# Kernel optimization log

Hardware: AMD Instinct MI355X
Metric: run time of the kernel (lower is better)

The kernel has to match this reference:

```python
import jax, jax.numpy as jnp
import numpy as np

HIDDEN = 1024
HEADS = 16
HEAD_DIM = HIDDEN // HEADS


def setup_inputs() -> dict:
    key = jax.random.key(0)
    ks = jax.random.split(key, 12)
    B, S, D = 2, 2048, HIDDEN
    scale = 1.0 / np.sqrt(D)
    return {
        "query": jax.random.normal(ks[0], (B, S, D), jnp.float32),
        "key": jax.random.normal(ks[1], (B, S, D), jnp.float32),
        "value": jax.random.normal(ks[2], (B, S, D), jnp.float32),
        "Wq": jax.random.normal(ks[3], (D, D), jnp.float32) * scale,
        "bq": jnp.zeros((D,), jnp.float32),
        "Wk": jax.random.normal(ks[4], (D, D), jnp.float32) * scale,
        "bk": jnp.zeros((D,), jnp.float32),
        "Wv": jax.random.normal(ks[5], (D, D), jnp.float32) * scale,
        "bv": jnp.zeros((D,), jnp.float32),
        "Wo": jax.random.normal(ks[6], (D, D), jnp.float32) * scale,
        "bo": jnp.zeros((D,), jnp.float32),
    }


def reference(query, key, value, Wq, bq, Wk, bk, Wv, bv, Wo, bo):
    B, S, D = query.shape
    H, Hd = HEADS, HEAD_DIM
    sm_scale = 1.0 / jnp.sqrt(jnp.asarray(Hd, query.dtype))

    def proj(x, W, b):  # nn.Linear: x @ W.T + b, then split heads -> [B,H,S,Hd]
        y = jnp.einsum("bsd,ed->bse", x, W) + b
        return y.reshape(B, S, H, Hd).transpose(0, 2, 1, 3)

    Q = proj(query, Wq, bq)
    K = proj(key, Wk, bk)
    V = proj(value, Wv, bv)

    scores = jnp.einsum("bhqd,bhkd->bhqk", Q, K) * sm_scale  # [B,H,S,S]
    attn = jax.nn.softmax(scores, axis=-1)
    ctx = jnp.einsum("bhqk,bhkd->bhqd", attn, V)
    ctx = ctx.transpose(0, 2, 1, 3).reshape(B, S, D)
    out = jnp.einsum("bsd,ed->bse", ctx, Wo) + bo
    return out
```

## Files before the change

kernel.cpp:

```cpp
#include <hip/hip_runtime.h>
#include <stdint.h>

typedef unsigned short u16;
typedef unsigned int u32;
typedef __attribute__((ext_vector_type(8))) short s16x8;
typedef __attribute__((ext_vector_type(4))) float fx4;

#define AS_GLOBAL __attribute__((address_space(1)))
#define AS_LDS    __attribute__((address_space(3)))

__device__ __forceinline__ void g2l16(const u16* g, u16* l) {
  __builtin_amdgcn_global_load_lds((const AS_GLOBAL unsigned int*)g,
                                   (AS_LDS unsigned int*)l, 16, 0, 0);
}
__device__ __forceinline__ u16 f2bf(float f) {
  u32 u = __float_as_uint(f);
  u += 0x7FFF + ((u >> 16) & 1);
  return (u16)(u >> 16);
}
__device__ __forceinline__ u32 pkcvt(float a, float b) {
  u32 r;
  asm("v_cvt_pk_bf16_f32 %0, %1, %2" : "=v"(r) : "v"(a), "v"(b));
  return r;
}

__global__ __launch_bounds__(256) void cvt3(const float* __restrict__ a, const float* __restrict__ b,
                                            const float* __restrict__ c, u16* oa, u16* ob, u16* oc, int n4) {
  const float* src = blockIdx.y == 0 ? a : blockIdx.y == 1 ? b : c;
  u16* dst = blockIdx.y == 0 ? oa : blockIdx.y == 1 ? ob : oc;
  int i = blockIdx.x * 256 + threadIdx.x;
  if (i >= n4) return;
  float4 f = ((const float4*)src)[i];
  ushort4 o; o.x = f2bf(f.x); o.y = f2bf(f.y); o.z = f2bf(f.z); o.w = f2bf(f.w);
  ((ushort4*)dst)[i] = o;
}
__global__ __launch_bounds__(256) void cvt4(const float* __restrict__ a, const float* __restrict__ b,
                                            const float* __restrict__ c, const float* __restrict__ d,
                                            u16* oa, u16* ob, u16* oc, u16* od, int n4) {
  const float* src = blockIdx.y == 0 ? a : blockIdx.y == 1 ? b : blockIdx.y == 2 ? c : d;
  u16* dst = blockIdx.y == 0 ? oa : blockIdx.y == 1 ? ob : blockIdx.y == 2 ? oc : od;
  int i = blockIdx.x * 256 + threadIdx.x;
  if (i >= n4) return;
  float4 f = ((const float4*)src)[i];
  ushort4 o; o.x = f2bf(f.x); o.y = f2bf(f.y); o.z = f2bf(f.z); o.w = f2bf(f.w);
  ((ushort4*)dst)[i] = o;
}

__global__ __launch_bounds__(256) void gemm_qkv(
    const u16* __restrict__ Aq, const u16* __restrict__ Ak, const u16* __restrict__ Av,
    const u16* __restrict__ Wq, const u16* __restrict__ Wk, const u16* __restrict__ Wv,
    const float* __restrict__ bq, const float* __restrict__ bk, const float* __restrict__ bv,
    u16* __restrict__ Oq, u16* __restrict__ Ok, u16* __restrict__ Ovt)
{
  constexpr int K = 1024;
  __shared__ u16 As[128 * 32];
  __shared__ u16 Bs[128 * 32];
  const int z = blockIdx.z;
  const u16* A = z == 0 ? Aq : z == 1 ? Ak : Av;
  const u16* W = z == 0 ? Wq : z == 1 ? Wk : Wv;
  const float* bias = z == 0 ? bq : z == 1 ? bk : bv;
  const float scale = z == 0 ? 0.180336880f : 1.0f;

  const int bm = blockIdx.x, bn = blockIdx.y;
  const int tid = threadIdx.x;
  const int lane = tid & 63, wave = tid >> 6;
  const int quad = lane >> 4, col = lane & 15;
  const int wm = wave >> 1, wn = wave & 1;

  const int L0 = tid, L1 = 256 + tid;
  const int r0 = L0 >> 2, c0 = (L0 & 3) ^ ((r0 >> 1) & 3);
  const int r1 = L1 >> 2, c1 = (L1 & 3) ^ ((r1 >> 1) & 3);
  const u16* gA0 = A + (bm * 128 + r0) * K + c0 * 8;
  const u16* gA1 = A + (bm * 128 + r1) * K + c1 * 8;
  const u16* gB0 = W + (bn * 128 + r0) * K + c0 * 8;
  const u16* gB1 = W + (bn * 128 + r1) * K + c1 * 8;
  u16* lA0 = As + L0 * 8; u16* lA1 = As + L1 * 8;
  u16* lB0 = Bs + L0 * 8; u16* lB1 = Bs + L1 * 8;

  const int aRow = wm * 64 + col;
  const int bRow = wn * 64 + col;

  fx4 zero = {0.f, 0.f, 0.f, 0.f};
  fx4 acc[4][4];
#pragma unroll
  for (int i = 0; i < 4; ++i)
#pragma unroll
    for (int j = 0; j < 4; ++j) acc[i][j] = zero;

  for (int kb = 0; kb < K / 32; ++kb) {
    __syncthreads();
    g2l16(gA0 + kb * 32, lA0);
    g2l16(gA1 + kb * 32, lA1);
    g2l16(gB0 + kb * 32, lB0);
    g2l16(gB1 + kb * 32, lB1);
    __syncthreads();
    s16x8 af[4], bf[4];
#pragma unroll
    for (int mt = 0; mt < 4; ++mt) {
      int row = aRow + mt * 16;
      int ch = row * 4 + (quad ^ ((row >> 1) & 3));
      af[mt] = *(const s16x8*)(As + ch * 8);
    }
#pragma unroll
    for (int nt = 0; nt < 4; ++nt) {
      int row = bRow + nt * 16;
      int ch = row * 4 + (quad ^ ((row >> 1) & 3));
      bf[nt] = *(const s16x8*)(Bs + ch * 8);
    }
#pragma unroll
    for (int mt = 0; mt < 4; ++mt)
#pragma unroll
      for (int nt = 0; nt < 4; ++nt)
        acc[mt][nt] = __builtin_amdgcn_mfma_f32_16x16x32_bf16(af[mt], bf[nt], acc[mt][nt], 0, 0, 0);
  }

  if (z == 2) {
#pragma unroll
    for (int nt = 0; nt < 4; ++nt) {
      int n = bn * 128 + wn * 64 + nt * 16 + col;
      float bvv = bias[n];
      int h = n >> 6, hd = n & 63;
#pragma unroll
      for (int mt = 0; mt < 4; ++mt) {
        int mbase = bm * 128 + wm * 64 + mt * 16 + quad * 4;
        int b = mbase >> 11, s = mbase & 2047;
        uint2 w;
        w.x = pkcvt(acc[mt][nt][0] + bvv, acc[mt][nt][1] + bvv);
        w.y = pkcvt(acc[mt][nt][2] + bvv, acc[mt][nt][3] + bvv);
        *(uint2*)(Ovt + ((size_t)((b * 16 + h) * 64 + hd)) * 2048 + s) = w;
      }
    }
  } else {
    u16* outB = z == 0 ? Oq : Ok;
#pragma unroll
    for (int nt = 0; nt < 4; ++nt) {
      int n = bn * 128 + wn * 64 + nt * 16 + col;
      float bvv = bias[n];
#pragma unroll
      for (int mt = 0; mt < 4; ++mt) {
        int mbase = bm * 128 + wm * 64 + mt * 16 + quad * 4;
#pragma unroll
        for (int reg = 0; reg < 4; ++reg) {
          int m = mbase + reg;
          float v = (acc[mt][nt][reg] + bvv) * scale;
          int b = m >> 11, s = m & 2047;
          int h = n >> 6, hd = n & 63;
          outB[((b * 16 + h) * 2048 + s) * 64 + hd] = f2bf(v);
        }
      }
    }
  }
}

__global__ __launch_bounds__(256) void gemm_out(
    const u16* __restrict__ A, const u16* __restrict__ W,
    const float* __restrict__ bias, float* __restrict__ outF)
{
  constexpr int K = 1024;
  __shared__ u16 As[128 * 32];
  __shared__ u16 Bs[64 * 32];
  const int bm = blockIdx.x, bn = blockIdx.y;
  const int tid = threadIdx.x;
  const int lane = tid & 63, wave = tid >> 6;
  const int quad = lane >> 4, col = lane & 15;
  const int wm = wave >> 1, wn = wave & 1;

  const int L0 = tid, L1 = 256 + tid;
  const int r0 = L0 >> 2, c0 = (L0 & 3) ^ ((r0 >> 1) & 3);
  const int r1 = L1 >> 2, c1 = (L1 & 3) ^ ((r1 >> 1) & 3);
  const u16* gA0 = A + (bm * 128 + r0) * K + c0 * 8;
  const u16* gA1 = A + (bm * 128 + r1) * K + c1 * 8;
  const u16* gB0 = W + (bn * 64 + r0) * K + c0 * 8;
  u16* lA0 = As + L0 * 8; u16* lA1 = As + L1 * 8;
  u16* lB0 = Bs + L0 * 8;

  const int aRow = wm * 64 + col;
  const int bRow = wn * 32 + col;

  fx4 zero = {0.f, 0.f, 0.f, 0.f};
  fx4 acc[4][2];
#pragma unroll
  for (int i = 0; i < 4; ++i)
#pragma unroll
    for (int j = 0; j < 2; ++j) acc[i][j] = zero;

  for (int kb = 0; kb < K / 32; ++kb) {
    __syncthreads();
    g2l16(gA0 + kb * 32, lA0);
    g2l16(gA1 + kb * 32, lA1);
    g2l16(gB0 + kb * 32, lB0);
    __syncthreads();
    s16x8 af[4], bf[2];
#pragma unroll
    for (int mt = 0; mt < 4; ++mt) {
      int row = aRow + mt * 16;
      int ch = row * 4 + (quad ^ ((row >> 1) & 3));
      af[mt] = *(const s16x8*)(As + ch * 8);
    }
#pragma unroll
    for (int nt = 0; nt < 2; ++nt) {
      int row = bRow + nt * 16;
      int ch = row * 4 + (quad ^ ((row >> 1) & 3));
      bf[nt] = *(const s16x8*)(Bs + ch * 8);
    }
#pragma unroll
    for (int mt = 0; mt < 4; ++mt)
#pragma unroll
      for (int nt = 0; nt < 2; ++nt)
        acc[mt][nt] = __builtin_amdgcn_mfma_f32_16x16x32_bf16(af[mt], bf[nt], acc[mt][nt], 0, 0, 0);
  }

#pragma unroll
  for (int nt = 0; nt < 2; ++nt) {
    int n = bn * 64 + wn * 32 + nt * 16 + col;
    float bvv = bias[n];
#pragma unroll
    for (int mt = 0; mt < 4; ++mt) {
      int mbase = bm * 128 + wm * 64 + mt * 16 + quad * 4;
#pragma unroll
      for (int reg = 0; reg < 4; ++reg)
        outF[(mbase + reg) * 1024 + n] = acc[mt][nt][reg] + bvv;
    }
  }
}

__global__ __launch_bounds__(512, 4) void flash_attn(
    const u16* __restrict__ Qp, const u16* __restrict__ Kp,
    const u16* __restrict__ Vt, u16* __restrict__ ctx)
{
  __shared__ u16 sh[32768];
  const int qt = blockIdx.x, bh = blockIdx.y;
  const int tid = threadIdx.x, lane = tid & 63, wave = tid >> 6;
  const int quad = lane >> 4, col = lane & 15;
  const int wm = wave >> 1, wn = wave & 1;

  const u16* Qb = Qp + ((size_t)bh * 2048 + qt * 128) * 64;
  const u16* Kb = Kp + (size_t)bh * 2048 * 64;
  const u16* Vb = Vt + (size_t)bh * 64 * 2048;

  s16x8 qf[2][2];
#pragma unroll
  for (int mt = 0; mt < 2; ++mt)
#pragma unroll
    for (int h = 0; h < 2; ++h)
      qf[mt][h] = *(const s16x8*)(Qb + (wm * 32 + mt * 16 + col) * 64 + h * 32 + quad * 8);

  fx4 zero = {0.f, 0.f, 0.f, 0.f};
  fx4 acc_o[2][4], acc_l[2];
#pragma unroll
  for (int mt = 0; mt < 2; ++mt) {
    acc_l[mt] = zero;
#pragma unroll
    for (int dt = 0; dt < 4; ++dt) acc_o[mt][dt] = zero;
  }
  s16x8 ones;
#pragma unroll
  for (int j = 0; j < 8; ++j) ones[j] = (short)0x3F80;

  u16* Vs = sh;
  u16* Ks = sh + 8192;
  u16* Pw = sh + 16384 + wave * 2048;

  const u16* vsrc[2];
#pragma unroll
  for (int i = 0; i < 2; ++i) {
    int d = wave * 8 + i * 4 + (lane >> 4);
    int cs = (lane & 15) ^ (d & 15);
    vsrc[i] = Vb + d * 2048 + cs * 8;
  }

  const u16* ksrc[2];
  u16* kdst[2];
#pragma unroll
  for (int i = 0; i < 2; ++i) {
    int idx = wave * 128 + i * 64 + lane;
    int d = idx >> 3, c = idx & 7;
    ksrc[i] = Kb + d * 64 + (c ^ (d & 7)) * 8;
    kdst[i] = Ks + (wave * 128 + i * 64) * 8;
  }

#pragma unroll
  for (int i = 0; i < 2; ++i) g2l16(ksrc[i], kdst[i]);
  asm volatile("s_waitcnt vmcnt(0)" ::: "memory");

  for (int kv = 0; kv < 16; ++kv) {
    const int n0 = kv * 128;
    __builtin_amdgcn_s_barrier();
#pragma unroll
    for (int i = 0; i < 2; ++i)
      g2l16(vsrc[i] + n0, Vs + (wave * 8 + i * 4) * 128);

    __builtin_amdgcn_s_setprio(1);
#pragma unroll
    for (int nt = 0; nt < 4; ++nt) {
      const int r = wn * 64 + nt * 16 + col;
      const u16* krow = Ks + r * 64;
      const int x = r & 7;
      s16x8 k0 = *(const s16x8*)(krow + ((quad ^ x) << 3));
      s16x8 k1 = *(const s16x8*)(krow + (((4 ^ quad) ^ x) << 3));
#pragma unroll
      for (int mt = 0; mt < 2; ++mt) {
        fx4 s = __builtin_amdgcn_mfma_f32_16x16x32_bf16(k0, qf[mt][0], zero, 0, 0, 0);
        s = __builtin_amdgcn_mfma_f32_16x16x32_bf16(k1, qf[mt][1], s, 0, 0, 0);
        int m = mt * 16 + col;
        int cch = 2 * nt + (quad >> 1);
        uint2 w;
        w.x = pkcvt(exp2f(s[0]), exp2f(s[1]));
        w.y = pkcvt(exp2f(s[2]), exp2f(s[3]));
        *(uint2*)(Pw + m * 64 + ((cch ^ (m & 7))) * 8 + (quad & 1) * 4) = w;
      }
    }
    __builtin_amdgcn_s_setprio(0);

    asm volatile("s_waitcnt vmcnt(0)" ::: "memory");
    asm volatile("s_waitcnt lgkmcnt(0)" ::: "memory");
    __builtin_amdgcn_s_barrier();

    if (kv < 15) {
#pragma unroll
      for (int i = 0; i < 2; ++i)
        g2l16(ksrc[i] + (kv + 1) * 8192, kdst[i]);
    }

    __builtin_amdgcn_s_setprio(1);
#pragma unroll
    for (int ks = 0; ks < 2; ++ks) {
      s16x8 pf[2];
#pragma unroll
      for (int mt = 0; mt < 2; ++mt)
        pf[mt] = *(const s16x8*)(Pw + (mt * 16 + col) * 64 + ((4 * ks + quad) ^ (col & 7)) * 8);
#pragma unroll
      for (int dt = 0; dt < 4; ++dt) {
        s16x8 vf = *(const s16x8*)(Vs + (dt * 16 + col) * 128 + ((wn * 8 + 4 * ks + quad) ^ col) * 8);
#pragma unroll
        for (int mt = 0; mt < 2; ++mt)
          acc_o[mt][dt] = __builtin_amdgcn_mfma_f32_16x16x32_bf16(pf[mt], vf, acc_o[mt][dt], 0, 0, 0);
      }
#pragma unroll
      for (int mt = 0; mt < 2; ++mt)
        acc_l[mt] = __builtin_amdgcn_mfma_f32_16x16x32_bf16(pf[mt], ones, acc_l[mt], 0, 0, 0);
    }
    __builtin_amdgcn_s_setprio(0);

    asm volatile("s_waitcnt vmcnt(0)" ::: "memory");
  }

  __syncthreads();
  float* buf = (float*)sh;
  if (wn == 1) {
#pragma unroll
    for (int mt = 0; mt < 2; ++mt) {
#pragma unroll
      for (int dt = 0; dt < 4; ++dt)
#pragma unroll
        for (int e = 0; e < 4; ++e)
          buf[wm * 2560 + ((mt * 4 + dt) * 4 + e) * 64 + lane] = acc_o[mt][dt][e];
#pragma unroll
      for (int e = 0; e < 4; ++e)
        buf[wm * 2560 + (32 + mt * 4 + e) * 64 + lane] = acc_l[mt][e];
    }
  }
  __syncthreads();
  if (wn == 0) {
    const int b = bh >> 4, h = bh & 15;
#pragma unroll
    for (int mt = 0; mt < 2; ++mt) {
      fx4 rl;
#pragma unroll
      for (int e = 0; e < 4; ++e) {
        float l = acc_l[mt][e] + buf[wm * 2560 + (32 + mt * 4 + e) * 64 + lane];
        rl[e] = 1.0f / l;
      }
#pragma unroll
      for (int dt = 0; dt < 4; ++dt)
#pragma unroll
        for (int e = 0; e < 4; ++e) {
          float v = (acc_o[mt][dt][e] + buf[wm * 2560 + ((mt * 4 + dt) * 4 + e) * 64 + lane]) * rl[e];
          int s = qt * 128 + wm * 32 + mt * 16 + quad * 4 + e;
          ctx[((size_t)(b * 2048 + s)) * 1024 + h * 64 + dt * 16 + col] = f2bf(v);
        }
    }
  }
}

extern "C" void kernel_launch(void* const* d_in, const int* in_sizes, int n_in,
                              void* d_out, int out_size, void* d_ws, size_t ws_size,
                              hipStream_t stream) {
  const float* q  = (const float*)d_in[0];
  const float* k  = (const float*)d_in[1];
  const float* v  = (const float*)d_in[2];
  const float* Wq = (const float*)d_in[3];
  const float* bq = (const float*)d_in[4];
  const float* Wk = (const float*)d_in[5];
  const float* bk = (const float*)d_in[6];
  const float* Wv = (const float*)d_in[7];
  const float* bv = (const float*)d_in[8];
  const float* Wo = (const float*)d_in[9];
  const float* bo = (const float*)d_in[10];
  float* out = (float*)d_out;

  char* ws = (char*)d_ws;
  const size_t MB = 1u << 20;
  u16* qb  = (u16*)(ws + 0 * MB);
  u16* kb  = (u16*)(ws + 8 * MB);
  u16* vb  = (u16*)(ws + 16 * MB);
  u16* wqb = (u16*)(ws + 24 * MB);
  u16* wkb = (u16*)(ws + 26 * MB);
  u16* wvb = (u16*)(ws + 28 * MB);
  u16* wob = (u16*)(ws + 30 * MB);
  u16* Qp  = (u16*)(ws + 32 * MB);
  u16* Kp  = (u16*)(ws + 40 * MB);
  u16* Vtp = (u16*)(ws + 56 * MB);
  u16* ctx = (u16*)(ws + 64 * MB);

  cvt3<<<dim3(4096, 3), 256, 0, stream>>>(q, k, v, qb, kb, vb, 1048576);
  cvt4<<<dim3(1024, 4), 256, 0, stream>>>(Wq, Wk, Wv, Wo, wqb, wkb, wvb, wob, 262144);

  gemm_qkv<<<dim3(32, 8, 3), 256, 0, stream>>>(qb, kb, vb, wqb, wkb, wvb,
                                               bq, bk, bv, Qp, Kp, Vtp);
  flash_attn<<<dim3(16, 32), 512, 0, stream>>>(Qp, Kp, Vtp, ctx);
  gemm_out<<<dim3(32, 16), 256, 0, stream>>>(ctx, wob, bo, out);
}
```

Before: 221.4 us.

## Double-buffer LDS in projection GEMMs and merge conversion kernels into one launch

Both projection GEMMs now use two LDS buffers, so the global-to-LDS loads for the next K tile are issued before computing the current one. This halves the barriers per tile and overlaps memory latency with MFMA work. The two fp32-to-bf16 conversion kernels are merged into one seven-slice launch, removing a kernel launch at the cost of many early-exit blocks for the weight slices. LDS use per block doubles, which may lower occupancy.

New measurement: 227.8 us. 1.03x slower.

```diff
diff --git a/kernel.cpp b/kernel.cpp
--- a/kernel.cpp
+++ b/kernel.cpp
@@ -24,23 +24,19 @@
   return r;
 }
 
-__global__ __launch_bounds__(256) void cvt3(const float* __restrict__ a, const float* __restrict__ b,
-                                            const float* __restrict__ c, u16* oa, u16* ob, u16* oc, int n4) {
-  const float* src = blockIdx.y == 0 ? a : blockIdx.y == 1 ? b : c;
-  u16* dst = blockIdx.y == 0 ? oa : blockIdx.y == 1 ? ob : oc;
+__global__ __launch_bounds__(256) void cvt7(
+    const float* __restrict__ q, const float* __restrict__ k, const float* __restrict__ v,
+    const float* __restrict__ Wq, const float* __restrict__ Wk,
+    const float* __restrict__ Wv, const float* __restrict__ Wo,
+    u16* qb, u16* kb, u16* vb, u16* wqb, u16* wkb, u16* wvb, u16* wob) {
+  const int y = blockIdx.y;
+  const int n4 = y < 3 ? 1048576 : 262144;
   int i = blockIdx.x * 256 + threadIdx.x;
   if (i >= n4) return;
-  float4 f = ((const float4*)src)[i];
-  ushort4 o; o.x = f2bf(f.x); o.y = f2bf(f.y); o.z = f2bf(f.z); o.w = f2bf(f.w);
-  ((ushort4*)dst)[i] = o;
-}
-__global__ __launch_bounds__(256) void cvt4(const float* __restrict__ a, const float* __restrict__ b,
-                                            const float* __restrict__ c, const float* __restrict__ d,
-                                            u16* oa, u16* ob, u16* oc, u16* od, int n4) {
-  const float* src = blockIdx.y == 0 ? a : blockIdx.y == 1 ? b : blockIdx.y == 2 ? c : d;
-  u16* dst = blockIdx.y == 0 ? oa : blockIdx.y == 1 ? ob : blockIdx.y == 2 ? oc : od;
-  int i = blockIdx.x * 256 + threadIdx.x;
-  if (i >= n4) return;
+  const float* src = y == 0 ? q : y == 1 ? k : y == 2 ? v
+                   : y == 3 ? Wq : y == 4 ? Wk : y == 5 ? Wv : Wo;
+  u16* dst = y == 0 ? qb : y == 1 ? kb : y == 2 ? vb
+           : y == 3 ? wqb : y == 4 ? wkb : y == 5 ? wvb : wob;
   float4 f = ((const float4*)src)[i];
   ushort4 o; o.x = f2bf(f.x); o.y = f2bf(f.y); o.z = f2bf(f.z); o.w = f2bf(f.w);
   ((ushort4*)dst)[i] = o;
@@ -53,8 +49,10 @@
     u16* __restrict__ Oq, u16* __restrict__ Ok, u16* __restrict__ Ovt)
 {
   constexpr int K = 1024;
-  __shared__ u16 As[128 * 32];
-  __shared__ u16 Bs[128 * 32];
+  __shared__ u16 As0[128 * 32];
+  __shared__ u16 Bs0[128 * 32];
+  __shared__ u16 As1[128 * 32];
+  __shared__ u16 Bs1[128 * 32];
   const int z = blockIdx.z;
   const u16* A = z == 0 ? Aq : z == 1 ? Ak : Av;
   const u16* W = z == 0 ? Wq : z == 1 ? Wk : Wv;
@@ -74,8 +72,6 @@
   const u16* gA1 = A + (bm * 128 + r1) * K + c1 * 8;
   const u16* gB0 = W + (bn * 128 + r0) * K + c0 * 8;
   const u16* gB1 = W + (bn * 128 + r1) * K + c1 * 8;
-  u16* lA0 = As + L0 * 8; u16* lA1 = As + L1 * 8;
-  u16* lB0 = Bs + L0 * 8; u16* lB1 = Bs + L1 * 8;
 
   const int aRow = wm * 64 + col;
   const int bRow = wn * 64 + col;
@@ -87,32 +83,45 @@
 #pragma unroll
     for (int j = 0; j < 4; ++j) acc[i][j] = zero;
 
-  for (int kb = 0; kb < K / 32; ++kb) {
+#define STAGE_QKV(AS, BS, kb)                 \
+  do {                                        \
+    g2l16(gA0 + (kb) * 32, (AS) + L0 * 8);    \
+    g2l16(gA1 + (kb) * 32, (AS) + L1 * 8);    \
+    g2l16(gB0 + (kb) * 32, (BS) + L0 * 8);    \
+    g2l16(gB1 + (kb) * 32, (BS) + L1 * 8);    \
+  } while (0)
+
+#define COMPUTE_QKV(AS, BS)                                                         \
+  do {                                                                              \
+    s16x8 af[4], bf[4];                                                             \
+    _Pragma("unroll") for (int mt = 0; mt < 4; ++mt) {                              \
+      int row = aRow + mt * 16;                                                     \
+      int ch = row * 4 + (quad ^ ((row >> 1) & 3));                                 \
+      af[mt] = *(const s16x8*)((AS) + ch * 8);                                      \
+    }                                                                               \
+    _Pragma("unroll") for (int nt = 0; nt < 4; ++nt) {                              \
+      int row = bRow + nt * 16;                                                     \
+      int ch = row * 4 + (quad ^ ((row >> 1) & 3));                                 \
+      bf[nt] = *(const s16x8*)((BS) + ch * 8);                                      \
+    }                                                                               \
+    _Pragma("unroll") for (int mt = 0; mt < 4; ++mt)                                \
+      _Pragma("unroll") for (int nt = 0; nt < 4; ++nt)                              \
+        acc[mt][nt] = __builtin_amdgcn_mfma_f32_16x16x32_bf16(af[mt], bf[nt],       \
+                                                              acc[mt][nt], 0, 0, 0);\
+  } while (0)
+
+  STAGE_QKV(As0, Bs0, 0);
+  __syncthreads();
+  for (int kb = 0; kb < K / 32; kb += 2) {
+    if (kb + 1 < K / 32) STAGE_QKV(As1, Bs1, kb + 1);
+    COMPUTE_QKV(As0, Bs0);
     __syncthreads();
-    g2l16(gA0 + kb * 32, lA0);
-    g2l16(gA1 + kb * 32, lA1);
-    g2l16(gB0 + kb * 32, lB0);
-    g2l16(gB1 + kb * 32, lB1);
+    if (kb + 2 < K / 32) STAGE_QKV(As0, Bs0, kb + 2);
+    COMPUTE_QKV(As1, Bs1);
     __syncthreads();
-    s16x8 af[4], bf[4];
-#pragma unroll
-    for (int mt = 0; mt < 4; ++mt) {
-      int row = aRow + mt * 16;
-      int ch = row * 4 + (quad ^ ((row >> 1) & 3));
-      af[mt] = *(const s16x8*)(As + ch * 8);
-    }
-#pragma unroll
-    for (int nt = 0; nt < 4; ++nt) {
-      int row = bRow + nt * 16;
-      int ch = row * 4 + (quad ^ ((row >> 1) & 3));
-      bf[nt] = *(const s16x8*)(Bs + ch * 8);
-    }
-#pragma unroll
-    for (int mt = 0; mt < 4; ++mt)
-#pragma unroll
-      for (int nt = 0; nt < 4; ++nt)
-        acc[mt][nt] = __builtin_amdgcn_mfma_f32_16x16x32_bf16(af[mt], bf[nt], acc[mt][nt], 0, 0, 0);
-  }
+  }
+#undef STAGE_QKV
+#undef COMPUTE_QKV
 
   if (z == 2) {
 #pragma unroll
@@ -157,8 +166,10 @@
     const float* __restrict__ bias, float* __restrict__ outF)
 {
   constexpr int K = 1024;
-  __shared__ u16 As[128 * 32];
-  __shared__ u16 Bs[64 * 32];
+  __shared__ u16 As0[128 * 32];
+  __shared__ u16 Bs0[64 * 32];
+  __shared__ u16 As1[128 * 32];
+  __shared__ u16 Bs1[64 * 32];
   const int bm = blockIdx.x, bn = blockIdx.y;
   const int tid = threadIdx.x;
   const int lane = tid & 63, wave = tid >> 6;
@@ -171,8 +182,6 @@
   const u16* gA0 = A + (bm * 128 + r0) * K + c0 * 8;
   const u16* gA1 = A + (bm * 128 + r1) * K + c1 * 8;
   const u16* gB0 = W + (bn * 64 + r0) * K + c0 * 8;
-  u16* lA0 = As + L0 * 8; u16* lA1 = As + L1 * 8;
-  u16* lB0 = Bs + L0 * 8;
 
   const int aRow = wm * 64 + col;
   const int bRow = wn * 32 + col;
@@ -184,31 +193,44 @@
 #pragma unroll
     for (int j = 0; j < 2; ++j) acc[i][j] = zero;
 
-  for (int kb = 0; kb < K / 32; ++kb) {
+#define STAGE_OUT(AS, BS, kb)                 \
+  do {                                        \
+    g2l16(gA0 + (kb) * 32, (AS) + L0 * 8);    \
+    g2l16(gA1 + (kb) * 32, (AS) + L1 * 8);    \
+    g2l16(gB0 + (kb) * 32, (BS) + L0 * 8);    \
+  } while (0)
+
+#define COMPUTE_OUT(AS, BS)                                                         \
+  do {                                                                              \
+    s16x8 af[4], bf[2];                                                             \
+    _Pragma("unroll") for (int mt = 0; mt < 4; ++mt) {                              \
+      int row = aRow + mt * 16;                                                     \
+      int ch = row * 4 + (quad ^ ((row >> 1) & 3));                                 \
+      af[mt] = *(const s16x8*)((AS) + ch * 8);                                      \
+    }                                                                               \
+    _Pragma("unroll") for (int nt = 0; nt < 2; ++nt) {                              \
+      int row = bRow + nt * 16;                                                     \
+      int ch = row * 4 + (quad ^ ((row >> 1) & 3));                                 \
+      bf[nt] = *(const s16x8*)((BS) + ch * 8);                                      \
+    }                                                                               \
+    _Pragma("unroll") for (int mt = 0; mt < 4; ++mt)                                \
+      _Pragma("unroll") for (int nt = 0; nt < 2; ++nt)                              \
+        acc[mt][nt] = __builtin_amdgcn_mfma_f32_16x16x32_bf16(af[mt], bf[nt],       \
+                                                              acc[mt][nt], 0, 0, 0);\
+  } while (0)
+
+  STAGE_OUT(As0, Bs0, 0);
+  __syncthreads();
+  for (int kb = 0; kb < K / 32; kb += 2) {
+    if (kb + 1 < K / 32) STAGE_OUT(As1, Bs1, kb + 1);
+    COMPUTE_OUT(As0, Bs0);
     __syncthreads();
-    g2l16(gA0 + kb * 32, lA0);
-    g2l16(gA1 + kb * 32, lA1);
-    g2l16(gB0 + kb * 32, lB0);
+    if (kb + 2 < K / 32) STAGE_OUT(As0, Bs0, kb + 2);
+    COMPUTE_OUT(As1, Bs1);
     __syncthreads();
-    s16x8 af[4], bf[2];
-#pragma unroll
-    for (int mt = 0; mt < 4; ++mt) {
-      int row = aRow + mt * 16;
-      int ch = row * 4 + (quad ^ ((row >> 1) & 3));
-      af[mt] = *(const s16x8*)(As + ch * 8);
-    }
-#pragma unroll
-    for (int nt = 0; nt < 2; ++nt) {
-      int row = bRow + nt * 16;
-      int ch = row * 4 + (quad ^ ((row >> 1) & 3));
-      bf[nt] = *(const s16x8*)(Bs + ch * 8);
-    }
-#pragma unroll
-    for (int mt = 0; mt < 4; ++mt)
-#pragma unroll
-      for (int nt = 0; nt < 2; ++nt)
-        acc[mt][nt] = __builtin_amdgcn_mfma_f32_16x16x32_bf16(af[mt], bf[nt], acc[mt][nt], 0, 0, 0);
-  }
+  }
+#undef STAGE_OUT
+#undef COMPUTE_OUT
 
 #pragma unroll
   for (int nt = 0; nt < 2; ++nt) {
@@ -413,8 +435,8 @@
   u16* Vtp = (u16*)(ws + 56 * MB);
   u16* ctx = (u16*)(ws + 64 * MB);
 
-  cvt3<<<dim3(4096, 3), 256, 0, stream>>>(q, k, v, qb, kb, vb, 1048576);
-  cvt4<<<dim3(1024, 4), 256, 0, stream>>>(Wq, Wk, Wv, Wo, wqb, wkb, wvb, wob, 262144);
+  cvt7<<<dim3(4096, 7), 256, 0, stream>>>(q, k, v, Wq, Wk, Wv, Wo,
+                                          qb, kb, vb, wqb, wkb, wvb, wob);
 
   gemm_qkv<<<dim3(32, 8, 3), 256, 0, stream>>>(qb, kb, vb, wqb, wkb, wvb,
                                                bq, bk, bv, Qp, Kp, Vtp);
```
